# Kernel optimization log

Measured on AMD Instinct MI355X. Metric: run time of the kernel, lower is better.

The kernel has to match this reference:

```python
import jax, jax.numpy as jnp
import numpy as np

H = W = 56; WS = 7; SHIFT = 3; NH = 6; DIM = 192; DEPTH = 2
HD = DIM // NH; NW = (H // WS) * (W // WS); N = WS * WS; SCALE = HD ** -0.5

# relative position index (constant, as in WindowAttention.__init__)
_c = np.stack(np.meshgrid(np.arange(WS), np.arange(WS), indexing='ij')).reshape(2, -1)
_r = (_c[:, :, None] - _c[:, None, :]).transpose(1, 2, 0)
_r[..., 0] += WS - 1; _r[..., 1] += WS - 1; _r[..., 0] *= 2 * WS - 1
RPI = jnp.asarray(_r.sum(-1).reshape(-1))  # (N*N,)

def _build_mask():
    # shifted-window attention mask (constant, built in SwinTransformerBlock.__init__)
    img = np.zeros((H, W))
    sl = (slice(0, -WS), slice(-WS, -SHIFT), slice(-SHIFT, None))
    cnt = 0
    for hs in sl:
        for ws_ in sl:
            img[hs, ws_] = cnt; cnt += 1
    mw = img.reshape(H // WS, WS, W // WS, WS).transpose(0, 2, 1, 3).reshape(-1, N)
    am = mw[:, None, :] - mw[:, :, None]  # (nW, N, N)
    return jnp.asarray(np.where(am != 0, -100.0, 0.0).astype(np.float32))

MASK = _build_mask()

def _ln(x, g, b):
    m = jnp.mean(x, -1, keepdims=True)
    v = jnp.mean((x - m) ** 2, -1, keepdims=True)
    return (x - m) * jax.lax.rsqrt(v + 1e-5) * g + b

def setup_inputs() -> dict:
    key = jax.random.key(0)
    ks = jax.random.split(key, 8)
    B = 64; s = 0.02
    return {
        'x': jax.random.normal(ks[0], (B, H * W, DIM), jnp.float32),
        'norm1_g': jnp.ones((DEPTH, DIM), jnp.float32),
        'norm1_b': jnp.zeros((DEPTH, DIM), jnp.float32),
        'qkv_w': jax.random.normal(ks[1], (DEPTH, DIM, 3 * DIM), jnp.float32) * s,
        'qkv_b': jnp.zeros((DEPTH, 3 * DIM), jnp.float32),
        'rpb': jax.random.normal(ks[2], (DEPTH, (2 * WS - 1) ** 2, NH), jnp.float32) * s,
        'proj_w': jax.random.normal(ks[3], (DEPTH, DIM, DIM), jnp.float32) * s,
        'proj_b': jnp.zeros((DEPTH, DIM), jnp.float32),
        'norm2_g': jnp.ones((DEPTH, DIM), jnp.float32),
        'norm2_b': jnp.zeros((DEPTH, DIM), jnp.float32),
        'fc1_w': jax.random.normal(ks[4], (DEPTH, DIM, 4 * DIM), jnp.float32) * s,
        'fc1_b': jnp.zeros((DEPTH, 4 * DIM), jnp.float32),
        'fc2_w': jax.random.normal(ks[5], (DEPTH, 4 * DIM, DIM), jnp.float32) * s,
        'fc2_b': jnp.zeros((DEPTH, DIM), jnp.float32),
    }

def reference(x, norm1_g, norm1_b, qkv_w, qkv_b, rpb, proj_w, proj_b,
              norm2_g, norm2_b, fc1_w, fc1_b, fc2_w, fc2_b):
    B = x.shape[0]
    for i in range(DEPTH):
        shift = 0 if i % 2 == 0 else WS // 2
        # --- windowed MHSA branch ---
        h = _ln(x, norm1_g[i], norm1_b[i]).reshape(B, H, W, DIM)
        if shift:
            h = jnp.roll(h, (-shift, -shift), (1, 2))
        # window partition -> (B*nW, N, C)
        w = h.reshape(B, H // WS, WS, W // WS, WS, DIM)
        w = w.transpose(0, 1, 3, 2, 4, 5).reshape(B * NW, N, DIM)
        qkv = (w @ qkv_w[i] + qkv_b[i]).reshape(B * NW, N, 3, NH, HD)
        qkv = qkv.transpose(2, 0, 3, 1, 4)  # (3, Bw, NH, N, HD)
        q, k, v = qkv[0] * SCALE, qkv[1], qkv[2]
        attn = jnp.einsum('bhnd,bhmd->bhnm', q, k)  # (Bw, NH, N, N)
        bias = rpb[i][RPI].reshape(N, N, NH).transpose(2, 0, 1)
        attn = attn + bias[None]
        if shift:
            attn = attn.reshape(B, NW, NH, N, N) + MASK[None, :, None]
            attn = attn.reshape(B * NW, NH, N, N)
        attn = jax.nn.softmax(attn, axis=-1)
        o = jnp.einsum('bhnm,bhmd->bhnd', attn, v)
        o = o.transpose(0, 2, 1, 3).reshape(B * NW, N, DIM)
        o = o @ proj_w[i] + proj_b[i]
        # window reverse
        h = o.reshape(B, H // WS, W // WS, WS, WS, DIM)
        h = h.transpose(0, 1, 3, 2, 4, 5).reshape(B, H, W, DIM)
        if shift:
            h = jnp.roll(h, (shift, shift), (1, 2))
        x = x + h.reshape(B, H * W, DIM)
        # --- MLP branch ---
        m = _ln(x, norm2_g[i], norm2_b[i])
        m = jax.nn.gelu(m @ fc1_w[i] + fc1_b[i], approximate=False)
        x = x + (m @ fc2_w[i] + fc2_b[i])
    return x
```

## Files before the change

### kernel.cpp

```cpp
#include <hip/hip_runtime.h>
#include <stdint.h>

#define NTOK   49
#define BATCH  64
#define MROWS  (BATCH * 64 * NTOK)
#define SCALE_ 0.17677669529663687f

typedef __attribute__((ext_vector_type(8))) short bf16x8;
typedef __attribute__((ext_vector_type(4))) float f32x4;

union V8 { uint4 u; unsigned short s[8]; };

__device__ __forceinline__ float bf2f(unsigned short u) {
  union { unsigned int i; float f; } c; c.i = ((unsigned int)u) << 16; return c.f;
}
__device__ __forceinline__ unsigned short f2bf(float f) {
  union { float f; unsigned int i; } c; c.f = f;
  unsigned int lsb = (c.i >> 16) & 1;
  return (unsigned short)((c.i + 0x7fffu + lsb) >> 16);
}

__global__ __launch_bounds__(256) void wt_k(const float* __restrict__ W,
    unsigned short* __restrict__ Wt, int K, int N)
{
  int idx = blockIdx.x * 256 + threadIdx.x;
  if (idx < K * N) {
    int k = idx / N, n = idx - k * N;
    Wt[(size_t)n * K + k] = f2bf(W[idx]);
  }
}

__global__ __launch_bounds__(256) void ln_k(const float* __restrict__ X,
    const float* __restrict__ g, const float* __restrict__ b,
    unsigned short* __restrict__ out, int shift)
{
  int wr = blockIdx.x * 4 + (threadIdx.x >> 6);
  int lane = threadIdx.x & 63;
  int win = wr / 49, n = wr % 49;
  int bi = win >> 6, w64 = win & 63;
  int wh = w64 >> 3, ww = w64 & 7;
  int ti = n / 7, tj = n % 7;
  int gh = wh * 7 + ti + shift; if (gh >= 56) gh -= 56;
  int gw = ww * 7 + tj + shift; if (gw >= 56) gw -= 56;
  size_t srow = (size_t)bi * 3136 + gh * 56 + gw;
  const float* xr = X + srow * 192;
  float v0 = xr[lane], v1 = xr[lane + 64], v2 = xr[lane + 128];
  float s  = v0 + v1 + v2;
  float s2 = v0*v0 + v1*v1 + v2*v2;
  #pragma unroll
  for (int m = 32; m >= 1; m >>= 1) { s += __shfl_xor(s, m); s2 += __shfl_xor(s2, m); }
  float mean = s * (1.0f/192.0f);
  float var  = s2 * (1.0f/192.0f) - mean*mean;
  float inv  = rsqrtf(var + 1e-5f);
  unsigned short* orow = out + (size_t)wr * 192;
  orow[lane]       = f2bf((v0-mean)*inv*g[lane]      + b[lane]);
  orow[lane+64]    = f2bf((v1-mean)*inv*g[lane+64]   + b[lane+64]);
  orow[lane+128]   = f2bf((v2-mean)*inv*g[lane+128]  + b[lane+128]);
}

template<int EPI>
__global__ __launch_bounds__(256) void gemm2_k(
    const unsigned short* __restrict__ A,
    const unsigned short* __restrict__ Wt,
    const float* __restrict__ bias,
    unsigned short* __restrict__ Cbf,
    const float* __restrict__ Xres,
    float* __restrict__ Xdst,
    int N, int shift)
{
  __shared__ unsigned short As[128][40];
  const int tid = threadIdx.x;
  const int lane = tid & 63, wv = tid >> 6;
  const int wm = wv >> 1, wn = wv & 1;
  const int row0 = blockIdx.x * 128;
  const int n0   = blockIdx.y * 64;
  f32x4 acc[4][2] = {};
  const int sr  = tid >> 1, ssg = (tid & 1) * 16;
  const int fr = lane & 15, kq = (lane >> 4) * 8;
  #pragma unroll
  for (int k0 = 0; k0 < 192; k0 += 32) {
    const uint4* asrc = reinterpret_cast<const uint4*>(A + (size_t)(row0 + sr) * 192 + k0 + ssg);
    uint4 av0 = asrc[0], av1 = asrc[1];
    __syncthreads();
    *reinterpret_cast<uint4*>(&As[sr][ssg])     = av0;
    *reinterpret_cast<uint4*>(&As[sr][ssg + 8]) = av1;
    __syncthreads();
    bf16x8 bfr[2];
    #pragma unroll
    for (int ni = 0; ni < 2; ++ni)
      bfr[ni] = *reinterpret_cast<const bf16x8*>(&Wt[(size_t)(n0 + wn*32 + ni*16 + fr) * 192 + k0 + kq]);
    #pragma unroll
    for (int mi = 0; mi < 4; ++mi) {
      bf16x8 afr = *reinterpret_cast<const bf16x8*>(&As[wm*64 + mi*16 + fr][kq]);
      #pragma unroll
      for (int ni = 0; ni < 2; ++ni)
        acc[mi][ni] = __builtin_amdgcn_mfma_f32_16x16x32_bf16(afr, bfr[ni], acc[mi][ni], 0, 0, 0);
    }
  }
  const int lcol = lane & 15, lr4 = (lane >> 4) * 4;
  #pragma unroll
  for (int mi = 0; mi < 4; ++mi)
  #pragma unroll
  for (int ni = 0; ni < 2; ++ni)
  #pragma unroll
  for (int i = 0; i < 4; ++i) {
    int gr = row0 + wm*64 + mi*16 + lr4 + i;
    int gc = n0 + wn*32 + ni*16 + lcol;
    float v = acc[mi][ni][i] + bias[gc];
    if (EPI == 0) {
      Cbf[(size_t)gr * N + gc] = f2bf(v);
    } else {
      int win = gr / 49, n = gr % 49;
      int bi = win >> 6, w64 = win & 63;
      int wh = w64 >> 3, ww = w64 & 7;
      int ti = n / 7, tj = n % 7;
      int gh = wh*7 + ti + shift; if (gh >= 56) gh -= 56;
      int gw = ww*7 + tj + shift; if (gw >= 56) gw -= 56;
      size_t idx = ((size_t)bi * 3136 + gh * 56 + gw) * 192 + gc;
      Xdst[idx] = Xres[idx] + v;
    }
  }
}

__global__ __launch_bounds__(512, 4) void mlp_k(
    const float* __restrict__ X,
    const float* __restrict__ g, const float* __restrict__ b,
    const unsigned short* __restrict__ W1t,
    const float* __restrict__ b1,
    const unsigned short* __restrict__ W2t,
    const float* __restrict__ b2,
    float* __restrict__ Y)
{
  __shared__ unsigned short As[64][200];
  __shared__ unsigned short Hs[64][396];
  const int row0 = blockIdx.x * 64;
  const int tid = threadIdx.x, lane = tid & 63, wv = tid >> 6;
  #pragma unroll
  for (int r = 0; r < 8; ++r) {
    int row = wv * 8 + r;
    const float* xr = X + (size_t)(row0 + row) * 192;
    float v0 = xr[lane], v1 = xr[lane + 64], v2 = xr[lane + 128];
    float s  = v0 + v1 + v2;
    float s2 = v0*v0 + v1*v1 + v2*v2;
    #pragma unroll
    for (int m = 32; m >= 1; m >>= 1) { s += __shfl_xor(s, m); s2 += __shfl_xor(s2, m); }
    float mean = s * (1.0f/192.0f);
    float var  = s2 * (1.0f/192.0f) - mean*mean;
    float inv  = rsqrtf(var + 1e-5f);
    As[row][lane]       = f2bf((v0-mean)*inv*g[lane]      + b[lane]);
    As[row][lane+64]    = f2bf((v1-mean)*inv*g[lane+64]   + b[lane+64]);
    As[row][lane+128]   = f2bf((v2-mean)*inv*g[lane+128]  + b[lane+128]);
  }
  __syncthreads();
  const int fr = lane & 15, kq = (lane >> 4) * 8;
  const int lcol = lane & 15, lr4 = (lane >> 4) * 4;
  const int wm2 = wv >> 2, wn2 = wv & 3;
  f32x4 acc2[2][3] = {};
  for (int hh = 0; hh < 2; ++hh) {
    f32x4 acc1[4][3] = {};
    const int c0 = hh * 384 + wv * 48;
    #pragma unroll
    for (int k0 = 0; k0 < 192; k0 += 32) {
      bf16x8 bfr[3];
      #pragma unroll
      for (int ni = 0; ni < 3; ++ni)
        bfr[ni] = *reinterpret_cast<const bf16x8*>(&W1t[(size_t)(c0 + ni*16 + fr) * 192 + k0 + kq]);
      #pragma unroll
      for (int mi = 0; mi < 4; ++mi) {
        bf16x8 afr = *reinterpret_cast<const bf16x8*>(&As[mi*16 + fr][k0 + kq]);
        #pragma unroll
        for (int ni = 0; ni < 3; ++ni)
          acc1[mi][ni] = __builtin_amdgcn_mfma_f32_16x16x32_bf16(afr, bfr[ni], acc1[mi][ni], 0, 0, 0);
      }
    }
    #pragma unroll
    for (int mi = 0; mi < 4; ++mi)
    #pragma unroll
    for (int ni = 0; ni < 3; ++ni)
    #pragma unroll
    for (int i = 0; i < 4; ++i) {
      int rr = mi*16 + lr4 + i;
      int cc = wv*48 + ni*16 + lcol;
      float v = acc1[mi][ni][i] + b1[hh*384 + cc];
      float gv = 0.5f * v * (1.0f + erff(v * 0.70710678118654752f));
      Hs[rr][cc] = f2bf(gv);
    }
    __syncthreads();
    #pragma unroll
    for (int k0 = 0; k0 < 384; k0 += 32) {
      bf16x8 bfr[3];
      #pragma unroll
      for (int ni = 0; ni < 3; ++ni)
        bfr[ni] = *reinterpret_cast<const bf16x8*>(&W2t[(size_t)(wn2*48 + ni*16 + fr) * 768 + hh*384 + k0 + kq]);
      #pragma unroll
      for (int mi = 0; mi < 2; ++mi) {
        bf16x8 afr = *reinterpret_cast<const bf16x8*>(&Hs[wm2*32 + mi*16 + fr][k0 + kq]);
        #pragma unroll
        for (int ni = 0; ni < 3; ++ni)
          acc2[mi][ni] = __builtin_amdgcn_mfma_f32_16x16x32_bf16(afr, bfr[ni], acc2[mi][ni], 0, 0, 0);
      }
    }
    __syncthreads();
  }
  #pragma unroll
  for (int mi = 0; mi < 2; ++mi)
  #pragma unroll
  for (int ni = 0; ni < 3; ++ni)
  #pragma unroll
  for (int i = 0; i < 4; ++i) {
    int grow = row0 + wm2*32 + mi*16 + lr4 + i;
    int gc = wn2*48 + ni*16 + lcol;
    float v = acc2[mi][ni][i] + b2[gc];
    size_t idx = (size_t)grow * 192 + gc;
    Y[idx] = X[idx] + v;
  }
}

template<bool SHIFTED>
__global__ __launch_bounds__(64) void attn_k(
    const unsigned short* __restrict__ qkv,
    const float* __restrict__ rpb,
    unsigned short* __restrict__ out)
{
  __shared__ float kv[2][49][32];
  int blk = blockIdx.x;
  int win = blk / 6, h = blk - win * 6;
  int lane = threadIdx.x;
  const unsigned short* base = qkv + (size_t)win * 49 * 576;
  for (int idx = lane; idx < 196; idx += 64) {
    int n = idx >> 2, sg = (idx & 3) * 8;
    V8 kk, vv;
    kk.u = *reinterpret_cast<const uint4*>(base + n*576 + 192 + h*32 + sg);
    vv.u = *reinterpret_cast<const uint4*>(base + n*576 + 384 + h*32 + sg);
    #pragma unroll
    for (int j = 0; j < 8; ++j) { kv[0][n][sg+j] = bf2f(kk.s[j]); kv[1][n][sg+j] = bf2f(vv.s[j]); }
  }
  __syncthreads();
  if (lane < 49) {
    float q[32];
    const unsigned short* qr = base + (size_t)lane * 576 + h * 32;
    #pragma unroll
    for (int sg = 0; sg < 4; ++sg) {
      V8 qq; qq.u = *reinterpret_cast<const uint4*>(qr + sg*8);
      #pragma unroll
      for (int j = 0; j < 8; ++j) q[sg*8+j] = bf2f(qq.s[j]) * SCALE_;
    }
    int ti = lane / 7, tj = lane - ti * 7;
    int wi = win & 63, wh = wi >> 3, ww = wi & 7;
    int rid = 0;
    if (SHIFTED) {
      int hh = wh*7 + ti, wg = ww*7 + tj;
      rid = (hh < 49 ? 0 : (hh < 53 ? 1 : 2)) * 3 + (wg < 49 ? 0 : (wg < 53 ? 1 : 2));
    }
    float s[49];
    float mx = -1e30f;
    #pragma unroll
    for (int m = 0; m < 49; ++m) {
      float a = 0.f;
      #pragma unroll
      for (int d4 = 0; d4 < 8; ++d4) {
        float4 kf = *reinterpret_cast<const float4*>(&kv[0][m][d4*4]);
        a += q[d4*4+0]*kf.x + q[d4*4+1]*kf.y + q[d4*4+2]*kf.z + q[d4*4+3]*kf.w;
      }
      int mi = m / 7, mj = m - mi * 7;
      a += rpb[((ti - mi + 6) * 13 + (tj - mj + 6)) * 6 + h];
      if (SHIFTED) {
        int hh = wh*7 + mi, wg = ww*7 + mj;
        int rid2 = (hh < 49 ? 0 : (hh < 53 ? 1 : 2)) * 3 + (wg < 49 ? 0 : (wg < 53 ? 1 : 2));
        if (rid2 != rid) a -= 100.f;
      }
      s[m] = a;
      mx = fmaxf(mx, a);
    }
    float sum = 0.f;
    #pragma unroll
    for (int m = 0; m < 49; ++m) { float e = __expf(s[m] - mx); s[m] = e; sum += e; }
    float rs = 1.f / sum;
    float o[32];
    #pragma unroll
    for (int d = 0; d < 32; ++d) o[d] = 0.f;
    #pragma unroll
    for (int m = 0; m < 49; ++m) {
      float p = s[m] * rs;
      #pragma unroll
      for (int d4 = 0; d4 < 8; ++d4) {
        float4 vf = *reinterpret_cast<const float4*>(&kv[1][m][d4*4]);
        o[d4*4+0] += p*vf.x; o[d4*4+1] += p*vf.y; o[d4*4+2] += p*vf.z; o[d4*4+3] += p*vf.w;
      }
    }
    unsigned short* orow = out + ((size_t)win * 49 + lane) * 192 + h * 32;
    #pragma unroll
    for (int sg = 0; sg < 4; ++sg) {
      V8 pk;
      #pragma unroll
      for (int j = 0; j < 8; ++j) pk.s[j] = f2bf(o[sg*8+j]);
      *reinterpret_cast<uint4*>(orow + sg*8) = pk.u;
    }
  }
}

extern "C" void kernel_launch(void* const* d_in, const int* in_sizes, int n_in,
                              void* d_out, int out_size, void* d_ws, size_t ws_size,
                              hipStream_t stream) {
  const float* x    = (const float*)d_in[0];
  const float* n1g  = (const float*)d_in[1];
  const float* n1b  = (const float*)d_in[2];
  const float* qkvw = (const float*)d_in[3];
  const float* qkvb = (const float*)d_in[4];
  const float* rpb  = (const float*)d_in[5];
  const float* pw   = (const float*)d_in[6];
  const float* pb   = (const float*)d_in[7];
  const float* n2g  = (const float*)d_in[8];
  const float* n2b  = (const float*)d_in[9];
  const float* f1w  = (const float*)d_in[10];
  const float* f1b  = (const float*)d_in[11];
  const float* f2w  = (const float*)d_in[12];
  const float* f2b  = (const float*)d_in[13];
  float* out = (float*)d_out;

  const size_t XBYTES = (size_t)MROWS * 192 * 4;
  const size_t ABYTES = (size_t)MROWS * 192 * 2;
  const size_t QBYTES = (size_t)MROWS * 576 * 2;
  char* ws = (char*)d_ws;
  float* x1 = (float*)ws;
  unsigned short* Abuf = (unsigned short*)(ws + XBYTES);
  unsigned short* Bbuf = (unsigned short*)(ws + XBYTES + ABYTES);
  unsigned short* WT   = (unsigned short*)(ws + XBYTES + ABYTES + QBYTES);
  const size_t WQ = 110592, WP = 36864, W1 = 147456, W2 = 147456;
  const size_t WD = WQ + WP + W1 + W2;

  for (int d = 0; d < 2; ++d) {
    unsigned short* wt = WT + d * WD;
    wt_k<<<(int)((WQ + 255)/256), 256, 0, stream>>>(qkvw + (size_t)d*WQ, wt,                 192, 576);
    wt_k<<<(int)((WP + 255)/256), 256, 0, stream>>>(pw   + (size_t)d*WP, wt + WQ,            192, 192);
    wt_k<<<(int)((W1 + 255)/256), 256, 0, stream>>>(f1w  + (size_t)d*W1, wt + WQ + WP,       192, 768);
    wt_k<<<(int)((W2 + 255)/256), 256, 0, stream>>>(f2w  + (size_t)d*W2, wt + WQ + WP + W1,  768, 192);
  }

  const int LNBLK = MROWS / 4;
  const dim3 G_QKV(MROWS/128, 9), G_P(MROWS/128, 3);

  for (int i = 0; i < 2; ++i) {
    int shift = i ? 3 : 0;
    const float* xin = i ? (const float*)x1 : x;
    float* xfin = i ? out : x1;
    const unsigned short* wt = WT + i * WD;
    ln_k<<<LNBLK, 256, 0, stream>>>(xin, n1g + i*192, n1b + i*192, Abuf, shift);
    gemm2_k<0><<<G_QKV, 256, 0, stream>>>(Abuf, wt, qkvb + i*576, Bbuf, nullptr, nullptr, 576, 0);
    if (shift) attn_k<true ><<<BATCH*64*6, 64, 0, stream>>>(Bbuf, rpb + i*169*6, Abuf);
    else       attn_k<false><<<BATCH*64*6, 64, 0, stream>>>(Bbuf, rpb + i*169*6, Abuf);
    gemm2_k<1><<<G_P, 256, 0, stream>>>(Abuf, wt + WQ, pb + i*192, nullptr, xin, x1, 192, shift);
    mlp_k<<<MROWS/64, 512, 0, stream>>>(x1, n2g + i*192, n2b + i*192,
                                        wt + WQ + WP, f1b + i*768,
                                        wt + WQ + WP + W1, f2b + i*192, xfin);
  }
}
```

Baseline: 1.882 ms.

## Preload weight fragments into registers in GEMM and retile MLP to 32-row blocks

The QKV/proj GEMM now loads all six K-steps of its B-fragments into registers up front and software-prefetches the next A tile while the current one is staged in LDS. The fused MLP kernel is retiled to 32-row blocks of 256 threads. It walks the hidden dimension in four 192-wide chunks, with per-chunk W1/W2 fragments held in registers, and the W2 loads are issued before the barrier so they overlap the GELU stores. This shrinks LDS per block and aims to hide global-load latency, at the cost of higher register pressure and twice as many MLP blocks, each reloading the weights.

Result: slower. 1.968 ms (+4.6%).

```diff
diff --git a/kernel.cpp b/kernel.cpp
--- a/kernel.cpp
+++ b/kernel.cpp
@@ -59,7 +59,7 @@
 }
 
 template<int EPI>
-__global__ __launch_bounds__(256) void gemm2_k(
+__global__ __launch_bounds__(256, 4) void gemm2_k(
     const unsigned short* __restrict__ A,
     const unsigned short* __restrict__ Wt,
     const float* __restrict__ bias,
@@ -74,27 +74,35 @@
   const int wm = wv >> 1, wn = wv & 1;
   const int row0 = blockIdx.x * 128;
   const int n0   = blockIdx.y * 64;
+  const int fr = lane & 15, kq = (lane >> 4) * 8;
+  bf16x8 bfr[6][2];
+  #pragma unroll
+  for (int ks = 0; ks < 6; ++ks)
+    #pragma unroll
+    for (int ni = 0; ni < 2; ++ni)
+      bfr[ks][ni] = *reinterpret_cast<const bf16x8*>(
+          &Wt[(size_t)(n0 + wn*32 + ni*16 + fr) * 192 + ks*32 + kq]);
+  const int sr  = tid >> 1, ssg = (tid & 1) * 16;
+  const unsigned short* arow = A + (size_t)(row0 + sr) * 192 + ssg;
+  uint4 a0 = *reinterpret_cast<const uint4*>(arow);
+  uint4 a1 = *reinterpret_cast<const uint4*>(arow + 8);
   f32x4 acc[4][2] = {};
-  const int sr  = tid >> 1, ssg = (tid & 1) * 16;
-  const int fr = lane & 15, kq = (lane >> 4) * 8;
-  #pragma unroll
-  for (int k0 = 0; k0 < 192; k0 += 32) {
-    const uint4* asrc = reinterpret_cast<const uint4*>(A + (size_t)(row0 + sr) * 192 + k0 + ssg);
-    uint4 av0 = asrc[0], av1 = asrc[1];
+  #pragma unroll
+  for (int ks = 0; ks < 6; ++ks) {
     __syncthreads();
-    *reinterpret_cast<uint4*>(&As[sr][ssg])     = av0;
-    *reinterpret_cast<uint4*>(&As[sr][ssg + 8]) = av1;
+    *reinterpret_cast<uint4*>(&As[sr][ssg])     = a0;
+    *reinterpret_cast<uint4*>(&As[sr][ssg + 8]) = a1;
+    if (ks < 5) {
+      a0 = *reinterpret_cast<const uint4*>(arow + (ks+1)*32);
+      a1 = *reinterpret_cast<const uint4*>(arow + (ks+1)*32 + 8);
+    }
     __syncthreads();
-    bf16x8 bfr[2];
-    #pragma unroll
-    for (int ni = 0; ni < 2; ++ni)
-      bfr[ni] = *reinterpret_cast<const bf16x8*>(&Wt[(size_t)(n0 + wn*32 + ni*16 + fr) * 192 + k0 + kq]);
     #pragma unroll
     for (int mi = 0; mi < 4; ++mi) {
       bf16x8 afr = *reinterpret_cast<const bf16x8*>(&As[wm*64 + mi*16 + fr][kq]);
       #pragma unroll
       for (int ni = 0; ni < 2; ++ni)
-        acc[mi][ni] = __builtin_amdgcn_mfma_f32_16x16x32_bf16(afr, bfr[ni], acc[mi][ni], 0, 0, 0);
+        acc[mi][ni] = __builtin_amdgcn_mfma_f32_16x16x32_bf16(afr, bfr[ks][ni], acc[mi][ni], 0, 0, 0);
     }
   }
   const int lcol = lane & 15, lr4 = (lane >> 4) * 4;
@@ -122,7 +130,7 @@
   }
 }
 
-__global__ __launch_bounds__(512, 4) void mlp_k(
+__global__ __launch_bounds__(256, 3) void mlp_k(
     const float* __restrict__ X,
     const float* __restrict__ g, const float* __restrict__ b,
     const unsigned short* __restrict__ W1t,
@@ -131,9 +139,9 @@
     const float* __restrict__ b2,
     float* __restrict__ Y)
 {
-  __shared__ unsigned short As[64][200];
-  __shared__ unsigned short Hs[64][396];
-  const int row0 = blockIdx.x * 64;
+  __shared__ unsigned short As[32][200];
+  __shared__ unsigned short Hs[32][200];
+  const int row0 = blockIdx.x * 32;
   const int tid = threadIdx.x, lane = tid & 63, wv = tid >> 6;
   #pragma unroll
   for (int r = 0; r < 8; ++r) {
@@ -154,53 +162,58 @@
   __syncthreads();
   const int fr = lane & 15, kq = (lane >> 4) * 8;
   const int lcol = lane & 15, lr4 = (lane >> 4) * 4;
-  const int wm2 = wv >> 2, wn2 = wv & 3;
   f32x4 acc2[2][3] = {};
-  for (int hh = 0; hh < 2; ++hh) {
-    f32x4 acc1[4][3] = {};
-    const int c0 = hh * 384 + wv * 48;
-    #pragma unroll
-    for (int k0 = 0; k0 < 192; k0 += 32) {
-      bf16x8 bfr[3];
+  #pragma unroll
+  for (int q = 0; q < 4; ++q) {
+    bf16x8 bw1[6][3];
+    #pragma unroll
+    for (int ks = 0; ks < 6; ++ks)
       #pragma unroll
       for (int ni = 0; ni < 3; ++ni)
-        bfr[ni] = *reinterpret_cast<const bf16x8*>(&W1t[(size_t)(c0 + ni*16 + fr) * 192 + k0 + kq]);
-      #pragma unroll
-      for (int mi = 0; mi < 4; ++mi) {
-        bf16x8 afr = *reinterpret_cast<const bf16x8*>(&As[mi*16 + fr][k0 + kq]);
+        bw1[ks][ni] = *reinterpret_cast<const bf16x8*>(
+            &W1t[(size_t)(q*192 + wv*48 + ni*16 + fr) * 192 + ks*32 + kq]);
+    f32x4 acc1[2][3] = {};
+    #pragma unroll
+    for (int ks = 0; ks < 6; ++ks) {
+      #pragma unroll
+      for (int mi = 0; mi < 2; ++mi) {
+        bf16x8 afr = *reinterpret_cast<const bf16x8*>(&As[mi*16 + fr][ks*32 + kq]);
         #pragma unroll
         for (int ni = 0; ni < 3; ++ni)
-          acc1[mi][ni] = __builtin_amdgcn_mfma_f32_16x16x32_bf16(afr, bfr[ni], acc1[mi][ni], 0, 0, 0);
-      }
-    }
-    #pragma unroll
-    for (int mi = 0; mi < 4; ++mi)
+          acc1[mi][ni] = __builtin_amdgcn_mfma_f32_16x16x32_bf16(afr, bw1[ks][ni], acc1[mi][ni], 0, 0, 0);
+      }
+    }
+    bf16x8 bw2[6][3];
+    #pragma unroll
+    for (int ks = 0; ks < 6; ++ks)
+      #pragma unroll
+      for (int ni = 0; ni < 3; ++ni)
+        bw2[ks][ni] = *reinterpret_cast<const bf16x8*>(
+            &W2t[(size_t)(wv*48 + ni*16 + fr) * 768 + q*192 + ks*32 + kq]);
+    __syncthreads();
+    #pragma unroll
+    for (int mi = 0; mi < 2; ++mi)
     #pragma unroll
     for (int ni = 0; ni < 3; ++ni)
     #pragma unroll
     for (int i = 0; i < 4; ++i) {
       int rr = mi*16 + lr4 + i;
       int cc = wv*48 + ni*16 + lcol;
-      float v = acc1[mi][ni][i] + b1[hh*384 + cc];
+      float v = acc1[mi][ni][i] + b1[q*192 + cc];
       float gv = 0.5f * v * (1.0f + erff(v * 0.70710678118654752f));
       Hs[rr][cc] = f2bf(gv);
     }
     __syncthreads();
     #pragma unroll
-    for (int k0 = 0; k0 < 384; k0 += 32) {
-      bf16x8 bfr[3];
-      #pragma unroll
-      for (int ni = 0; ni < 3; ++ni)
-        bfr[ni] = *reinterpret_cast<const bf16x8*>(&W2t[(size_t)(wn2*48 + ni*16 + fr) * 768 + hh*384 + k0 + kq]);
+    for (int ks = 0; ks < 6; ++ks) {
       #pragma unroll
       for (int mi = 0; mi < 2; ++mi) {
-        bf16x8 afr = *reinterpret_cast<const bf16x8*>(&Hs[wm2*32 + mi*16 + fr][k0 + kq]);
+        bf16x8 afr = *reinterpret_cast<const bf16x8*>(&Hs[mi*16 + fr][ks*32 + kq]);
         #pragma unroll
         for (int ni = 0; ni < 3; ++ni)
-          acc2[mi][ni] = __builtin_amdgcn_mfma_f32_16x16x32_bf16(afr, bfr[ni], acc2[mi][ni], 0, 0, 0);
-      }
-    }
-    __syncthreads();
+          acc2[mi][ni] = __builtin_amdgcn_mfma_f32_16x16x32_bf16(afr, bw2[ks][ni], acc2[mi][ni], 0, 0, 0);
+      }
+    }
   }
   #pragma unroll
   for (int mi = 0; mi < 2; ++mi)
@@ -208,8 +221,8 @@
   for (int ni = 0; ni < 3; ++ni)
   #pragma unroll
   for (int i = 0; i < 4; ++i) {
-    int grow = row0 + wm2*32 + mi*16 + lr4 + i;
-    int gc = wn2*48 + ni*16 + lcol;
+    int grow = row0 + mi*16 + lr4 + i;
+    int gc = wv*48 + ni*16 + lcol;
     float v = acc2[mi][ni][i] + b2[gc];
     size_t idx = (size_t)grow * 192 + gc;
     Y[idx] = X[idx] + v;
@@ -350,7 +363,7 @@
     if (shift) attn_k<true ><<<BATCH*64*6, 64, 0, stream>>>(Bbuf, rpb + i*169*6, Abuf);
     else       attn_k<false><<<BATCH*64*6, 64, 0, stream>>>(Bbuf, rpb + i*169*6, Abuf);
     gemm2_k<1><<<G_P, 256, 0, stream>>>(Abuf, wt + WQ, pb + i*192, nullptr, xin, x1, 192, shift);
-    mlp_k<<<MROWS/64, 512, 0, stream>>>(x1, n2g + i*192, n2b + i*192,
+    mlp_k<<<MROWS/32, 256, 0, stream>>>(x1, n2g + i*192, n2b + i*192,
                                         wt + WQ + WP, f1b + i*768,
                                         wt + WQ + WP + W1, f2b + i*192, xfin);
   }
```
